# Kernel tuning notes

Hardware: AMD Instinct MI355X
Metric: run time of the kernel (lower is better)

Reference implementation:

```python
import jax, jax.numpy as jnp
import numpy as np

B, S, D = 8, 2048, 512

def setup_inputs() -> dict:
    key = jax.random.key(0)
    k1, k2 = jax.random.split(key)
    lstm_out = jax.random.normal(k1, (B, S, D), dtype=jnp.float32)
    # xavier_uniform init for [D, D]
    limit = float(np.sqrt(6.0 / (D + D)))
    attention_weights = jax.random.uniform(k2, (D, D), dtype=jnp.float32, minval=-limit, maxval=limit)
    return {"lstm_out": lstm_out, "attention_weights": attention_weights}

def reference(lstm_out, attention_weights):
    # scores[b,i,j] = tanh( (x W) x^T )
    proj = jnp.einsum('bsd,de->bse', lstm_out, attention_weights)          # [B,S,D]
    scores = jnp.tanh(jnp.einsum('bsd,btd->bst', proj, lstm_out))          # [B,S,S]
    attn = jax.nn.softmax(scores, axis=-1)                                 # [B,S,S]
    return jnp.einsum('bst,btd->bsd', attn, lstm_out)                      # [B,S,D]
```

## Files before the change

### kernel.cpp

```cpp
#include <hip/hip_runtime.h>
#include <hip/hip_bf16.h>

typedef __bf16 bf16;
typedef __attribute__((ext_vector_type(8))) __bf16 bf16x8;
typedef __attribute__((ext_vector_type(4))) float floatx4;

__device__ __forceinline__ void gl_lds16(const bf16* g, bf16* l) {
    __builtin_amdgcn_global_load_lds(
        (const __attribute__((address_space(1))) unsigned int*)g,
        (__attribute__((address_space(3))) unsigned int*)l,
        16, 0, 0);
}

__global__ __launch_bounds__(256) void cast_both(const float* __restrict__ in,
                                                 bf16* __restrict__ outn,
                                                 bf16* __restrict__ outt,
                                                 int R, int C) {
    __shared__ float tile[32][33];
    const long long bz = blockIdx.z;
    in   += bz * (long long)R * C;
    outn += bz * (long long)R * C;
    outt += bz * (long long)R * C;
    const int r0 = blockIdx.x * 32, c0 = blockIdx.y * 32;
    const int tx = threadIdx.x & 31, ty = threadIdx.x >> 5;
#pragma unroll
    for (int i = 0; i < 32; i += 8) {
        float v = in[(long long)(r0 + ty + i) * C + (c0 + tx)];
        tile[ty + i][tx] = v;
        outn[(long long)(r0 + ty + i) * C + (c0 + tx)] = (bf16)v;
    }
    __syncthreads();
#pragma unroll
    for (int i = 0; i < 32; i += 8)
        outt[(long long)(c0 + ty + i) * R + (r0 + tx)] = (bf16)tile[tx][ty + i];
}

__global__ __launch_bounds__(256) void cast_transpose(const float* __restrict__ in,
                                                      bf16* __restrict__ out,
                                                      int R, int C) {
    __shared__ float tile[32][33];
    const int r0 = blockIdx.x * 32, c0 = blockIdx.y * 32;
    const int tx = threadIdx.x & 31, ty = threadIdx.x >> 5;
#pragma unroll
    for (int i = 0; i < 32; i += 8)
        tile[ty + i][tx] = in[(long long)(r0 + ty + i) * C + (c0 + tx)];
    __syncthreads();
#pragma unroll
    for (int i = 0; i < 32; i += 8)
        out[(long long)(c0 + ty + i) * R + (r0 + tx)] = (bf16)tile[tx][ty + i];
}

__device__ __forceinline__ float exp_tanh(float x) {
    float u = __expf(2.0f * x);
    float t = 1.0f - 2.0f / (u + 1.0f);
    float p = 1.0f / 720.0f;
    p = fmaf(p, t, 1.0f / 120.0f);
    p = fmaf(p, t, 1.0f / 24.0f);
    p = fmaf(p, t, 1.0f / 6.0f);
    p = fmaf(p, t, 0.5f);
    p = fmaf(p, t, 1.0f);
    p = fmaf(p, t, 1.0f);
    return p;
}

template <int MODE>
__global__ __launch_bounds__(256) void gemm128(const bf16* __restrict__ A,
                                               const bf16* __restrict__ Bm,
                                               void* __restrict__ Cout,
                                               float* __restrict__ rowsum,
                                               int M, int N, int K,
                                               long long batchA, long long batchB,
                                               long long batchC, long long batchR) {
    const long long bz = blockIdx.z;
    A  += bz * batchA;
    Bm += bz * batchB;

    __shared__ bf16 As[128 * 64];
    __shared__ bf16 Bs[128 * 64];
    __shared__ float rs[128];

    const int t    = threadIdx.x;
    const int lane = t & 63;
    const int wave = t >> 6;
    const int quad = lane >> 4;
    const int l16  = lane & 15;

    const int m0 = blockIdx.x * 128;
    const int n0 = blockIdx.y * 128;
    const int wm = (wave >> 1) * 64;
    const int wn = (wave & 1) * 64;

    floatx4 acc[4][4] = {};

    const int ra = t >> 3;
    const int ca = (((t & 7) ^ (ra & 7))) * 8;
    const long long rstep = 32LL * K;
    const bf16* Abase = A + (long long)(m0 + ra) * K + ca;
    const bf16* Bbase = Bm + (long long)(n0 + ra) * K + ca;

    const int cq0 = ((quad) ^ (l16 & 7)) * 8;
    const int cq1 = ((4 + quad) ^ (l16 & 7)) * 8;

    for (int k0 = 0; k0 < K; k0 += 64) {
#pragma unroll
        for (int i = 0; i < 4; ++i) {
            gl_lds16(Abase + k0 + i * rstep, &As[(t + 256 * i) * 8]);
            gl_lds16(Bbase + k0 + i * rstep, &Bs[(t + 256 * i) * 8]);
        }
        __syncthreads();

#pragma unroll
        for (int s = 0; s < 2; ++s) {
            const int cq = s ? cq1 : cq0;
            bf16x8 af[4], bfr[4];
#pragma unroll
            for (int i = 0; i < 4; ++i)
                af[i] = *(const bf16x8*)(&As[(wm + i * 16 + l16) * 64 + cq]);
#pragma unroll
            for (int j = 0; j < 4; ++j)
                bfr[j] = *(const bf16x8*)(&Bs[(wn + j * 16 + l16) * 64 + cq]);
#pragma unroll
            for (int i = 0; i < 4; ++i)
#pragma unroll
                for (int j = 0; j < 4; ++j)
                    acc[i][j] = __builtin_amdgcn_mfma_f32_16x16x32_bf16(af[i], bfr[j], acc[i][j], 0, 0, 0);
        }
        __syncthreads();
    }

    if (MODE == 1) {
        bf16* Cg = (bf16*)Cout + bz * batchC;
#pragma unroll
        for (int i = 0; i < 4; ++i)
#pragma unroll
            for (int r = 0; r < 4; ++r) {
                long long row = m0 + wm + i * 16 + quad * 4 + r;
                float s = 0.f;
#pragma unroll
                for (int j = 0; j < 4; ++j) {
                    float v = exp_tanh(acc[i][j][r]);
                    s += v;
                    Cg[row * (long long)N + (n0 + wn + j * 16 + l16)] = (bf16)v;
                }
#pragma unroll
                for (int msk = 1; msk < 16; msk <<= 1) s += __shfl_xor(s, msk);
                if (l16 == 0)
                    atomicAdd(&rowsum[bz * batchR + row], s);
            }
    } else {
        if (t < 128) rs[t] = rowsum[bz * batchR + m0 + t];
        __syncthreads();
        float* Og = (float*)Cout + bz * batchC;
#pragma unroll
        for (int i = 0; i < 4; ++i)
#pragma unroll
            for (int r = 0; r < 4; ++r) {
                int rl = wm + i * 16 + quad * 4 + r;
                float inv = 1.0f / rs[rl];
                long long row = m0 + rl;
#pragma unroll
                for (int j = 0; j < 4; ++j)
                    Og[row * (long long)N + (n0 + wn + j * 16 + l16)] = acc[i][j][r] * inv;
            }
    }
}

__global__ __launch_bounds__(256) void gemm64_nt(const bf16* __restrict__ A,
                                                 const bf16* __restrict__ Bm,
                                                 bf16* __restrict__ Cout,
                                                 int M, int N, int K) {
    __shared__ bf16 As[64 * 64];
    __shared__ bf16 Bs[128 * 64];

    const int t    = threadIdx.x;
    const int lane = t & 63;
    const int wave = t >> 6;
    const int quad = lane >> 4;
    const int l16  = lane & 15;

    const int m0 = blockIdx.x * 64;
    const int n0 = blockIdx.y * 128;
    const int wn = wave * 32;

    floatx4 acc[4][2] = {};

    const int ra = t >> 3;
    const int ca = (((t & 7) ^ (ra & 7))) * 8;
    const long long rstep = 32LL * K;
    const bf16* Abase = A + (long long)(m0 + ra) * K + ca;
    const bf16* Bbase = Bm + (long long)(n0 + ra) * K + ca;

    const int cq0 = ((quad) ^ (l16 & 7)) * 8;
    const int cq1 = ((4 + quad) ^ (l16 & 7)) * 8;

    for (int k0 = 0; k0 < K; k0 += 64) {
#pragma unroll
        for (int i = 0; i < 2; ++i)
            gl_lds16(Abase + k0 + i * rstep, &As[(t + 256 * i) * 8]);
#pragma unroll
        for (int i = 0; i < 4; ++i)
            gl_lds16(Bbase + k0 + i * rstep, &Bs[(t + 256 * i) * 8]);
        __syncthreads();

#pragma unroll
        for (int s = 0; s < 2; ++s) {
            const int cq = s ? cq1 : cq0;
            bf16x8 af[4], bfr[2];
#pragma unroll
            for (int i = 0; i < 4; ++i)
                af[i] = *(const bf16x8*)(&As[(i * 16 + l16) * 64 + cq]);
#pragma unroll
            for (int j = 0; j < 2; ++j)
                bfr[j] = *(const bf16x8*)(&Bs[(wn + j * 16 + l16) * 64 + cq]);
#pragma unroll
            for (int i = 0; i < 4; ++i)
#pragma unroll
                for (int j = 0; j < 2; ++j)
                    acc[i][j] = __builtin_amdgcn_mfma_f32_16x16x32_bf16(af[i], bfr[j], acc[i][j], 0, 0, 0);
        }
        __syncthreads();
    }

    bf16* Cg = Cout;
#pragma unroll
    for (int i = 0; i < 4; ++i)
#pragma unroll
        for (int r = 0; r < 4; ++r) {
            long long row = m0 + i * 16 + quad * 4 + r;
#pragma unroll
            for (int j = 0; j < 2; ++j)
                Cg[row * (long long)N + (n0 + wn + j * 16 + l16)] = (bf16)acc[i][j][r];
        }
}

extern "C" void kernel_launch(void* const* d_in, const int* in_sizes, int n_in,
                              void* d_out, int out_size, void* d_ws, size_t ws_size,
                              hipStream_t stream) {
    const int B = 8, S = 2048, D = 512;
    const float* x = (const float*)d_in[0];
    const float* W = (const float*)d_in[1];
    float* out = (float*)d_out;

    const size_t nx = (size_t)B * S * D;
    const size_t nw = (size_t)D * D;

    char* ws = (char*)d_ws;
    auto al = [](size_t v) { return (v + 255) & ~(size_t)255; };
    size_t off = 0;
    bf16* xb = (bf16*)(ws + off); off = al(off + nx * 2);
    bf16* xt = (bf16*)(ws + off); off = al(off + nx * 2);
    bf16* pb = (bf16*)(ws + off); off = al(off + nx * 2);
    bf16* wt = (bf16*)(ws + off); off = al(off + nw * 2);
    float* rsum = (float*)(ws + off); off = al(off + (size_t)B * S * 4);
    bf16* sb = (bf16*)(ws + off);
    const size_t full_need = off + (size_t)B * S * S * 2;
    const bool batched = (ws_size >= full_need);

    hipMemsetAsync(rsum, 0, (size_t)B * S * 4, stream);

    { dim3 g(S / 32, D / 32, B); cast_both<<<g, 256, 0, stream>>>(x, xb, xt, S, D); }
    { dim3 g(D / 32, D / 32, 1); cast_transpose<<<g, 256, 0, stream>>>(W, wt, D, D); }

    {
        dim3 g(B * S / 64, D / 128, 1);
        gemm64_nt<<<g, 256, 0, stream>>>(xb, wt, pb, B * S, D, D);
    }

    const long long sd = (long long)S * D;
    const long long ss = (long long)S * S;

    if (batched) {
        dim3 g2(S / 128, S / 128, B);
        gemm128<1><<<g2, 256, 0, stream>>>(pb, xb, (void*)sb, rsum, S, S, D, sd, sd, ss, S);
        dim3 g4(S / 128, D / 128, B);
        gemm128<2><<<g4, 256, 0, stream>>>(sb, xt, (void*)out, rsum, S, D, S, ss, sd, sd, S);
    } else {
        for (int b = 0; b < B; ++b) {
            dim3 g2(S / 128, S / 128, 1);
            gemm128<1><<<g2, 256, 0, stream>>>(pb + (size_t)b * sd, xb + (size_t)b * sd,
                                               (void*)sb, rsum + (size_t)b * S, S, S, D, 0, 0, 0, 0);
            dim3 g4(S / 128, D / 128, 1);
            gemm128<2><<<g4, 256, 0, stream>>>(sb, xt + (size_t)b * sd,
                                               (void*)(out + (size_t)b * sd), rsum + (size_t)b * S,
                                               S, D, S, 0, 0, 0, 0);
        }
    }
}
```

Before: 218.5 us.

## Replace atomic row sums with per-slot partials and swizzle tile order

The score GEMM now writes each wave's per-row exp sum into its own slot of a partial-sum buffer instead of doing atomicAdd. That removes the memset launch and atomic contention. The output GEMM sums the 32 slots and takes the reciprocal before its K loop. Both GEMMs also remap block indices into 4x2 groups to improve L2 reuse. The polynomial exp(tanh) is replaced by __expf of a fast tanh, which costs one more transcendental per element but has fewer FMAs.

```diff
diff --git a/kernel.cpp b/kernel.cpp
--- a/kernel.cpp
+++ b/kernel.cpp
@@ -4,12 +4,24 @@
 typedef __bf16 bf16;
 typedef __attribute__((ext_vector_type(8))) __bf16 bf16x8;
 typedef __attribute__((ext_vector_type(4))) float floatx4;
+
+#define NPART 16
+#define NSLOT 32
 
 __device__ __forceinline__ void gl_lds16(const bf16* g, bf16* l) {
     __builtin_amdgcn_global_load_lds(
         (const __attribute__((address_space(1))) unsigned int*)g,
         (__attribute__((address_space(3))) unsigned int*)l,
         16, 0, 0);
+}
+
+__device__ __forceinline__ void swizzle_mn(int& bm, int& bn) {
+    int gx = gridDim.x;
+    int f  = blockIdx.y * gx + blockIdx.x;
+    int st = f >> 3, r = f & 7;
+    int mgroups = gx >> 2;
+    bm = (st % mgroups) * 4 + (r & 3);
+    bn = (st / mgroups) * 2 + (r >> 2);
 }
 
 __global__ __launch_bounds__(256) void cast_both(const float* __restrict__ in,
@@ -50,24 +62,16 @@
         out[(long long)(c0 + ty + i) * R + (r0 + tx)] = (bf16)tile[tx][ty + i];
 }
 
-__device__ __forceinline__ float exp_tanh(float x) {
-    float u = __expf(2.0f * x);
-    float t = 1.0f - 2.0f / (u + 1.0f);
-    float p = 1.0f / 720.0f;
-    p = fmaf(p, t, 1.0f / 120.0f);
-    p = fmaf(p, t, 1.0f / 24.0f);
-    p = fmaf(p, t, 1.0f / 6.0f);
-    p = fmaf(p, t, 0.5f);
-    p = fmaf(p, t, 1.0f);
-    p = fmaf(p, t, 1.0f);
-    return p;
+__device__ __forceinline__ float fast_tanh(float v) {
+    float e = __expf(2.0f * v);
+    return 1.0f - 2.0f / (e + 1.0f);
 }
 
 template <int MODE>
 __global__ __launch_bounds__(256) void gemm128(const bf16* __restrict__ A,
                                                const bf16* __restrict__ Bm,
                                                void* __restrict__ Cout,
-                                               float* __restrict__ rowsum,
+                                               float* __restrict__ rpart,
                                                int M, int N, int K,
                                                long long batchA, long long batchB,
                                                long long batchC, long long batchR) {
@@ -85,8 +89,10 @@
     const int quad = lane >> 4;
     const int l16  = lane & 15;
 
-    const int m0 = blockIdx.x * 128;
-    const int n0 = blockIdx.y * 128;
+    int bm, bn;
+    swizzle_mn(bm, bn);
+    const int m0 = bm * 128;
+    const int n0 = bn * 128;
     const int wm = (wave >> 1) * 64;
     const int wn = (wave & 1) * 64;
 
@@ -101,6 +107,19 @@
     const int cq0 = ((quad) ^ (l16 & 7)) * 8;
     const int cq1 = ((4 + quad) ^ (l16 & 7)) * 8;
 
+    if (MODE == 2) {
+        if (t < 128) {
+            const float* pp = rpart + (bz * batchR + m0 + t) * NSLOT;
+            float s = 0.f;
+#pragma unroll
+            for (int c = 0; c < NSLOT / 4; ++c) {
+                float4 p = ((const float4*)pp)[c];
+                s += (p.x + p.y) + (p.z + p.w);
+            }
+            rs[t] = 1.0f / s;
+        }
+    }
+
     for (int k0 = 0; k0 < K; k0 += 64) {
 #pragma unroll
         for (int i = 0; i < 4; ++i) {
@@ -130,6 +149,7 @@
 
     if (MODE == 1) {
         bf16* Cg = (bf16*)Cout + bz * batchC;
+        const int slot = bn * 2 + (wave & 1);
 #pragma unroll
         for (int i = 0; i < 4; ++i)
 #pragma unroll
@@ -138,25 +158,23 @@
                 float s = 0.f;
 #pragma unroll
                 for (int j = 0; j < 4; ++j) {
-                    float v = exp_tanh(acc[i][j][r]);
+                    float v = __expf(fast_tanh(acc[i][j][r]));
                     s += v;
                     Cg[row * (long long)N + (n0 + wn + j * 16 + l16)] = (bf16)v;
                 }
 #pragma unroll
                 for (int msk = 1; msk < 16; msk <<= 1) s += __shfl_xor(s, msk);
                 if (l16 == 0)
-                    atomicAdd(&rowsum[bz * batchR + row], s);
+                    rpart[(bz * batchR + row) * NSLOT + slot] = s;
             }
     } else {
-        if (t < 128) rs[t] = rowsum[bz * batchR + m0 + t];
-        __syncthreads();
         float* Og = (float*)Cout + bz * batchC;
 #pragma unroll
         for (int i = 0; i < 4; ++i)
 #pragma unroll
             for (int r = 0; r < 4; ++r) {
                 int rl = wm + i * 16 + quad * 4 + r;
-                float inv = 1.0f / rs[rl];
+                float inv = rs[rl];
                 long long row = m0 + rl;
 #pragma unroll
                 for (int j = 0; j < 4; ++j)
@@ -221,7 +239,6 @@
         __syncthreads();
     }
 
-    bf16* Cg = Cout;
 #pragma unroll
     for (int i = 0; i < 4; ++i)
 #pragma unroll
@@ -229,7 +246,7 @@
             long long row = m0 + i * 16 + quad * 4 + r;
 #pragma unroll
             for (int j = 0; j < 2; ++j)
-                Cg[row * (long long)N + (n0 + wn + j * 16 + l16)] = (bf16)acc[i][j][r];
+                Cout[row * (long long)N + (n0 + wn + j * 16 + l16)] = (bf16)acc[i][j][r];
         }
 }
 
@@ -251,13 +268,11 @@
     bf16* xt = (bf16*)(ws + off); off = al(off + nx * 2);
     bf16* pb = (bf16*)(ws + off); off = al(off + nx * 2);
     bf16* wt = (bf16*)(ws + off); off = al(off + nw * 2);
-    float* rsum = (float*)(ws + off); off = al(off + (size_t)B * S * 4);
+    float* rpart = (float*)(ws + off); off = al(off + (size_t)B * S * NSLOT * 4);
     bf16* sb = (bf16*)(ws + off);
     const size_t full_need = off + (size_t)B * S * S * 2;
     const bool batched = (ws_size >= full_need);
 
-    hipMemsetAsync(rsum, 0, (size_t)B * S * 4, stream);
-
     { dim3 g(S / 32, D / 32, B); cast_both<<<g, 256, 0, stream>>>(x, xb, xt, S, D); }
     { dim3 g(D / 32, D / 32, 1); cast_transpose<<<g, 256, 0, stream>>>(W, wt, D, D); }
 
@@ -271,18 +286,19 @@
 
     if (batched) {
         dim3 g2(S / 128, S / 128, B);
-        gemm128<1><<<g2, 256, 0, stream>>>(pb, xb, (void*)sb, rsum, S, S, D, sd, sd, ss, S);
+        gemm128<1><<<g2, 256, 0, stream>>>(pb, xb, (void*)sb, rpart, S, S, D, sd, sd, ss, S);
         dim3 g4(S / 128, D / 128, B);
-        gemm128<2><<<g4, 256, 0, stream>>>(sb, xt, (void*)out, rsum, S, D, S, ss, sd, sd, S);
+        gemm128<2><<<g4, 256, 0, stream>>>(sb, xt, (void*)out, rpart, S, D, S, ss, sd, sd, S);
     } else {
         for (int b = 0; b < B; ++b) {
             dim3 g2(S / 128, S / 128, 1);
             gemm128<1><<<g2, 256, 0, stream>>>(pb + (size_t)b * sd, xb + (size_t)b * sd,
-                                               (void*)sb, rsum + (size_t)b * S, S, S, D, 0, 0, 0, 0);
+                                               (void*)sb, rpart + (size_t)b * S * NSLOT,
+                                               S, S, D, 0, 0, 0, S);
             dim3 g4(S / 128, D / 128, 1);
             gemm128<2><<<g4, 256, 0, stream>>>(sb, xt + (size_t)b * sd,
-                                               (void*)(out + (size_t)b * sd), rsum + (size_t)b * S,
-                                               S, D, S, 0, 0, 0, 0);
-        }
-    }
-}
+                                               (void*)(out + (size_t)b * sd), rpart + (size_t)b * S * NSLOT,
+                                               S, D, S, 0, 0, 0, S);
+        }
+    }
+}
```

Measured after the change: 209.5 us. -4.2%, faster.
